# Kernel optimization log

Hardware: AMD Instinct MI355X
Metric: run time of the kernel (lower is better)

The kernel has to match this reference:

```python
import jax, jax.numpy as jnp
import numpy as np

H, W = 256, 256
DX, DY = 1.0, 1.0
EI, KC, GC = 1.0, 1.0, 1.0
LAYERS = [2, 256, 512, 1024, H * W]
B = 64


def _d2x(f, dx):
    # reflect-pad width 1 on x (last axis), stencil [1, -2, 1]
    p = jnp.pad(f, ((0, 0), (0, 0), (0, 0), (1, 1)), mode='reflect')
    return (p[..., :-2] - 2.0 * p[..., 1:-1] + p[..., 2:]) / (dx * dx)


def _d2y(f, dy):
    p = jnp.pad(f, ((0, 0), (0, 0), (1, 1), (0, 0)), mode='reflect')
    return (p[:, :, :-2, :] - 2.0 * p[:, :, 1:-1, :] + p[:, :, 2:, :]) / (dy * dy)


def setup_inputs() -> dict:
    key = jax.random.key(0)
    ks = jax.random.split(key, 10)
    inp = {
        'x_coloc': jax.random.normal(ks[0], (B, LAYERS[0]), jnp.float32),
        'P': jax.random.normal(ks[1], (B, H * W), jnp.float32),
    }
    for i in range(4):
        inp[f'W{i + 1}'] = jax.random.normal(ks[2 + i], (LAYERS[i], LAYERS[i + 1]), jnp.float32) / np.sqrt(LAYERS[i]).astype(np.float32)
        inp[f'b{i + 1}'] = jnp.zeros((LAYERS[i + 1],), jnp.float32)
    return inp


def reference(x_coloc, P, W1, b1, W2, b2, W3, b3, W4, b4):
    # MLP field predictor: Linear+ReLU x3, final Linear -> [B, H*W]
    h = jax.nn.relu(x_coloc @ W1 + b1)
    h = jax.nn.relu(h @ W2 + b2)
    h = jax.nn.relu(h @ W3 + b3)
    f = h @ W4 + b4                      # [B, H*W]
    fm = f.reshape(B, 1, H, W)

    fx2 = _d2x(fm, DX)                   # d2/dx2
    fy2 = _d2y(fm, DY)                   # d2/dy2
    lap = fx2 + fy2
    biharmonic = _d2x(lap, DX) + _d2y(lap, DY)

    residual = EI * biharmonic + GC * (fx2 + fy2) + KC * fm - P.reshape(B, 1, H, W)
    return residual.reshape(B, H * W)
```

## Files before the change

kernel.cpp:

```cpp
#include <hip/hip_runtime.h>
#include <hip/hip_bf16.h>


#define BATCH 64
#define NPIX 65536

typedef __attribute__((ext_vector_type(8))) short short8_t;
typedef __attribute__((ext_vector_type(4))) float f32x4;

__device__ __forceinline__ short f2bf(float x) {
    __hip_bfloat16 h = __float2bfloat16(x);
    short s;
    __builtin_memcpy(&s, &h, 2);
    return s;
}

__global__ void k_layer12(const float* __restrict__ x, const float* __restrict__ W1,
                          const float* __restrict__ b1, const float* __restrict__ W2,
                          const float* __restrict__ b2, float* __restrict__ h2) {
    __shared__ float As[16][64];
    __shared__ float Ws[64][16];
    int tid = threadIdx.x;
    int tn = tid & 15, tm = tid >> 4;
    int n0 = blockIdx.x * 16, m0 = blockIdx.y * 16;
    float acc = 0.f;
    for (int k0 = 0; k0 < 256; k0 += 64) {
#pragma unroll
        for (int j = 0; j < 4; ++j) {
            int e = j * 256 + tid;
            int m = m0 + (e >> 6), kk = k0 + (e & 63);
            float v = x[m * 2 + 0] * W1[kk] + x[m * 2 + 1] * W1[256 + kk] + b1[kk];
            As[e >> 6][e & 63] = v > 0.f ? v : 0.f;
        }
#pragma unroll
        for (int j = 0; j < 4; ++j) {
            int e = j * 256 + tid;
            Ws[e >> 4][e & 15] = W2[(k0 + (e >> 4)) * 512 + n0 + (e & 15)];
        }
        __syncthreads();
#pragma unroll
        for (int k = 0; k < 64; ++k)
            acc += As[tm][k] * Ws[k][tn];
        __syncthreads();
    }
    acc += b2[n0 + tn];
    acc = acc > 0.f ? acc : 0.f;
    h2[(m0 + tm) * 512 + n0 + tn] = acc;
}

__global__ void k_layer3(const float* __restrict__ A, const float* __restrict__ Wt,
                         const float* __restrict__ bias, short* __restrict__ out_bf) {
    __shared__ float As[16][64];
    __shared__ float Ws[64][16];
    int tid = threadIdx.x;
    int tn = tid & 15, tm = tid >> 4;
    int n0 = blockIdx.x * 16, m0 = blockIdx.y * 16;
    float acc = 0.f;
    for (int k0 = 0; k0 < 512; k0 += 64) {
#pragma unroll
        for (int j = 0; j < 4; ++j) {
            int e = j * 256 + tid;
            As[e >> 6][e & 63] = A[(m0 + (e >> 6)) * 512 + k0 + (e & 63)];
        }
#pragma unroll
        for (int j = 0; j < 4; ++j) {
            int e = j * 256 + tid;
            Ws[e >> 4][e & 15] = Wt[(k0 + (e >> 4)) * 1024 + n0 + (e & 15)];
        }
        __syncthreads();
#pragma unroll
        for (int k = 0; k < 64; ++k)
            acc += As[tm][k] * Ws[k][tn];
        __syncthreads();
    }
    acc += bias[n0 + tn];
    acc = acc > 0.f ? acc : 0.f;
    out_bf[(m0 + tm) * 1024 + n0 + tn] = f2bf(acc);
}

__global__ __launch_bounds__(256) void k_gemm_mfma(
        const short* __restrict__ A,
        const float* __restrict__ W,
        const float* __restrict__ bias,
        float* __restrict__ f) {
    __shared__ float Wt[2][32 * 128];
    __shared__ short At[2][4 * 64 * 8];
    const int tid = threadIdx.x;
    const int w = tid >> 6;
    const int lane = tid & 63;
    const int lr = lane & 15;
    const int g = lane >> 4;
    const int n0 = blockIdx.x * 128;

    f32x4 acc[4][2];
#pragma unroll
    for (int a = 0; a < 4; ++a)
#pragma unroll
        for (int b = 0; b < 2; ++b)
            acc[a][b] = {0.f, 0.f, 0.f, 0.f};

    auto stage = [&](int b, int s) {
#pragma unroll
        for (int i = 0; i < 4; ++i) {
            int c = i * 256 + tid;
            int k = c >> 5;
            int q4 = (c & 31) * 4;
            int csw = q4 ^ (((k >> 3) & 1) << 4);
            const float* src = W + (size_t)(s * 32 + k) * NPIX + n0 + csw;
            __builtin_amdgcn_global_load_lds(
                (const __attribute__((address_space(1))) void*)src,
                (__attribute__((address_space(3))) void*)((char*)&Wt[b][0] + c * 16),
                16, 0, 0);
        }
        {
            int kq = tid >> 6;
            int ms = tid & 63;
            int md = ms ^ (kq << 2);
            const short* asrc = A + md * 1024 + s * 32 + kq * 8;
            __builtin_amdgcn_global_load_lds(
                (const __attribute__((address_space(1))) void*)asrc,
                (__attribute__((address_space(3))) void*)((char*)&At[b][0] + tid * 16),
                16, 0, 0);
        }
    };

    stage(0, 0);

    for (int s = 0; s < 32; ++s) {
        const int cur = s & 1;
        if (s < 31) {
            stage(cur ^ 1, s + 1);
            asm volatile("s_waitcnt vmcnt(5)" ::: "memory");
        } else {
            asm volatile("s_waitcnt vmcnt(0)" ::: "memory");
        }
        __builtin_amdgcn_sched_barrier(0);
        __builtin_amdgcn_s_barrier();
        __builtin_amdgcn_sched_barrier(0);

        short8_t afr[4];
#pragma unroll
        for (int mt = 0; mt < 4; ++mt) {
            int mrow = mt * 16 + lr;
            afr[mt] = *(const short8_t*)((const short*)&At[cur][0] +
                                         g * 512 + (mrow ^ (g << 2)) * 8);
        }
#pragma unroll
        for (int t = 0; t < 2; ++t) {
            const int col = w * 32 + t * 16 + lr;
            const int csw = col ^ ((g & 1) << 4);
            short8_t bfr;
#pragma unroll
            for (int j = 0; j < 8; ++j)
                bfr[j] = f2bf(Wt[cur][(g * 8 + j) * 128 + csw]);
#pragma unroll
            for (int mt = 0; mt < 4; ++mt)
                acc[mt][t] = __builtin_amdgcn_mfma_f32_16x16x32_bf16(afr[mt], bfr, acc[mt][t], 0, 0, 0);
        }
        __builtin_amdgcn_s_barrier();
    }

    __syncthreads();
    float* Cl = (float*)&Wt[0][0];
#pragma unroll
    for (int t = 0; t < 2; ++t) {
        const int colb = w * 32 + t * 16 + lr;
        float bb = bias[n0 + colb];
#pragma unroll
        for (int mt = 0; mt < 4; ++mt)
#pragma unroll
            for (int r = 0; r < 4; ++r)
                Cl[(mt * 16 + g * 4 + r) * 128 + colb] = acc[mt][t][r] + bb;
    }
    __syncthreads();
#pragma unroll
    for (int it = 0; it < 8; ++it) {
        int row = (tid >> 5) + it * 8;
        int cc = (tid & 31) * 4;
        f32x4 v = *(const f32x4*)&Cl[row * 128 + cc];
        *(f32x4*)(f + (size_t)row * NPIX + n0 + cc) = v;
    }
}

#define ROWS 16
__device__ __forceinline__ int rfl(int i) {
    return i < 0 ? -i : (i > 255 ? 510 - i : i);
}
__global__ void k_stencil(const float* __restrict__ f, const float* __restrict__ P,
                          float* __restrict__ out) {
    __shared__ float fs[ROWS + 4][256];
    __shared__ float ls[ROWS + 2][256];
    int x = threadIdx.x;
    int y0 = blockIdx.x * ROWS;
    int b = blockIdx.y;
    const float* fb = f + (size_t)b * NPIX;
#pragma unroll
    for (int t = 0; t < ROWS + 4; ++t) {
        int gy = rfl(y0 - 2 + t);
        fs[t][x] = fb[gy * 256 + x];
    }
    __syncthreads();

    int xm = x == 0 ? 1 : x - 1;
    int xp = x == 255 ? 254 : x + 1;

#pragma unroll
    for (int t = 0; t < ROWS + 2; ++t) {
        int jj = rfl(y0 - 1 + t);
        int s  = jj - y0 + 2;
        int sm = rfl(jj - 1) - y0 + 2;
        int sp = rfl(jj + 1) - y0 + 2;
        float c = fs[s][x];
        ls[t][x] = (fs[sm][x] - 2.f * c + fs[sp][x]) +
                   (fs[s][xm] - 2.f * c + fs[s][xp]);
    }
    __syncthreads();

#pragma unroll
    for (int r = 0; r < ROWS; ++r) {
        int y = y0 + r;
        float lc = ls[r + 1][x];
        float bih = (ls[r][x] - 2.f * lc + ls[r + 2][x]) +
                    (ls[r + 1][xm] - 2.f * lc + ls[r + 1][xp]);
        float fc = fs[r + 2][x];
        size_t idx = (size_t)b * NPIX + y * 256 + x;
        out[idx] = bih + lc + fc - P[idx];
    }
}

extern "C" void kernel_launch(void* const* d_in, const int* in_sizes, int n_in,
                              void* d_out, int out_size, void* d_ws, size_t ws_size,
                              hipStream_t stream) {
    const float* x  = (const float*)d_in[0];
    const float* P  = (const float*)d_in[1];
    const float* W1 = (const float*)d_in[2];
    const float* b1 = (const float*)d_in[3];
    const float* W2 = (const float*)d_in[4];
    const float* b2 = (const float*)d_in[5];
    const float* W3 = (const float*)d_in[6];
    const float* b3 = (const float*)d_in[7];
    const float* W4 = (const float*)d_in[8];
    const float* b4 = (const float*)d_in[9];
    float* out = (float*)d_out;

    char* ws = (char*)d_ws;
    float* h2  = (float*)(ws);
    short* h3b = (short*)(ws + (128 << 10));
    float* f   = (float*)(ws + (256 << 10));

    k_layer12<<<dim3(512 / 16, 4), 256, 0, stream>>>(x, W1, b1, W2, b2, h2);
    k_layer3<<<dim3(1024 / 16, 4), 256, 0, stream>>>(h2, W3, b3, h3b);
    k_gemm_mfma<<<NPIX / 128, 256, 0, stream>>>(h3b, W4, b4, f);
    k_stencil<<<dim3(256 / ROWS, BATCH), 256, 0, stream>>>(f, P, out);
}
```

Before: 81.97 us.

## Load A fragments directly to registers and double K-step in W4 GEMM

The large W4 GEMM kernel stops staging the bf16 activation tile through LDS and instead loads A fragments straight from global memory into registers, with a next-step register buffer. The K step per pipeline stage is doubled to 64, halving the number of iterations and barriers, and each stage is split into two halves with finer vmcnt waits so compute on the first half can start while the second half's W loads are still landing. This adds register pressure and doubles LDS use for W, which may reduce occupancy.

After: 88.28 us. 1.08x slower.

```diff
diff --git a/kernel.cpp b/kernel.cpp
--- a/kernel.cpp
+++ b/kernel.cpp
@@ -83,8 +83,7 @@
         const float* __restrict__ W,
         const float* __restrict__ bias,
         float* __restrict__ f) {
-    __shared__ float Wt[2][32 * 128];
-    __shared__ short At[2][4 * 64 * 8];
+    __shared__ float Wt[2][64 * 128];
     const int tid = threadIdx.x;
     const int w = tid >> 6;
     const int lane = tid & 63;
@@ -99,68 +98,89 @@
         for (int b = 0; b < 2; ++b)
             acc[a][b] = {0.f, 0.f, 0.f, 0.f};
 
-    auto stage = [&](int b, int s) {
-#pragma unroll
-        for (int i = 0; i < 4; ++i) {
+    const short* ap = A + lr * 1024 + g * 8;
+    short8_t aC[4][2], aN[4][2];
+
+    auto loadA = [&](short8_t (&dst)[4][2], int s) {
+#pragma unroll
+        for (int mt = 0; mt < 4; ++mt)
+#pragma unroll
+            for (int ks = 0; ks < 2; ++ks)
+                dst[mt][ks] = *(const short8_t*)(ap + mt * 16384 + s * 64 + ks * 32);
+    };
+
+    auto stageW = [&](int b, int s, int ilo, int ihi) {
+#pragma unroll
+        for (int i = 0; i < 8; ++i) {
+            if (i < ilo || i >= ihi) continue;
             int c = i * 256 + tid;
             int k = c >> 5;
             int q4 = (c & 31) * 4;
             int csw = q4 ^ (((k >> 3) & 1) << 4);
-            const float* src = W + (size_t)(s * 32 + k) * NPIX + n0 + csw;
+            const float* src = W + (size_t)(s * 64 + k) * NPIX + n0 + csw;
             __builtin_amdgcn_global_load_lds(
                 (const __attribute__((address_space(1))) void*)src,
                 (__attribute__((address_space(3))) void*)((char*)&Wt[b][0] + c * 16),
                 16, 0, 0);
         }
-        {
-            int kq = tid >> 6;
-            int ms = tid & 63;
-            int md = ms ^ (kq << 2);
-            const short* asrc = A + md * 1024 + s * 32 + kq * 8;
-            __builtin_amdgcn_global_load_lds(
-                (const __attribute__((address_space(1))) void*)asrc,
-                (__attribute__((address_space(3))) void*)((char*)&At[b][0] + tid * 16),
-                16, 0, 0);
-        }
     };
 
-    stage(0, 0);
-
-    for (int s = 0; s < 32; ++s) {
+    auto computeHalf = [&](int cur, int ks, short8_t (&aa)[4][2]) {
+#pragma unroll
+        for (int t = 0; t < 2; ++t) {
+            const int csw = (w * 32 + t * 16 + lr) ^ ((g & 1) << 4);
+            short8_t bfr;
+#pragma unroll
+            for (int j = 0; j < 8; ++j)
+                bfr[j] = f2bf(Wt[cur][(ks * 32 + g * 8 + j) * 128 + csw]);
+#pragma unroll
+            for (int mt = 0; mt < 4; ++mt)
+                acc[mt][t] = __builtin_amdgcn_mfma_f32_16x16x32_bf16(aa[mt][ks], bfr, acc[mt][t], 0, 0, 0);
+        }
+    };
+
+    loadA(aC, 0);
+    __builtin_amdgcn_sched_barrier(0);
+    stageW(0, 0, 0, 8);
+    __builtin_amdgcn_sched_barrier(0);
+
+    for (int s = 0; s < 16; ++s) {
         const int cur = s & 1;
-        if (s < 31) {
-            stage(cur ^ 1, s + 1);
-            asm volatile("s_waitcnt vmcnt(5)" ::: "memory");
+        if (s < 15) {
+            loadA(aN, s + 1);
+            __builtin_amdgcn_sched_barrier(0);
+            stageW(cur ^ 1, s + 1, 0, 4);
+            __builtin_amdgcn_sched_barrier(0);
+            stageW(cur ^ 1, s + 1, 4, 8);
+            __builtin_amdgcn_sched_barrier(0);
+            asm volatile("s_waitcnt vmcnt(20)" ::: "memory");
         } else {
+            asm volatile("s_waitcnt vmcnt(4)" ::: "memory");
+        }
+        __builtin_amdgcn_sched_barrier(0);
+        __builtin_amdgcn_s_barrier();
+        __builtin_amdgcn_sched_barrier(0);
+        computeHalf(cur, 0, aC);
+        if (s < 15)
+            asm volatile("s_waitcnt vmcnt(16)" ::: "memory");
+        else
             asm volatile("s_waitcnt vmcnt(0)" ::: "memory");
-        }
         __builtin_amdgcn_sched_barrier(0);
         __builtin_amdgcn_s_barrier();
         __builtin_amdgcn_sched_barrier(0);
-
-        short8_t afr[4];
-#pragma unroll
-        for (int mt = 0; mt < 4; ++mt) {
-            int mrow = mt * 16 + lr;
-            afr[mt] = *(const short8_t*)((const short*)&At[cur][0] +
-                                         g * 512 + (mrow ^ (g << 2)) * 8);
-        }
-#pragma unroll
-        for (int t = 0; t < 2; ++t) {
-            const int col = w * 32 + t * 16 + lr;
-            const int csw = col ^ ((g & 1) << 4);
-            short8_t bfr;
-#pragma unroll
-            for (int j = 0; j < 8; ++j)
-                bfr[j] = f2bf(Wt[cur][(g * 8 + j) * 128 + csw]);
+        computeHalf(cur, 1, aC);
+        if (s < 15) {
 #pragma unroll
             for (int mt = 0; mt < 4; ++mt)
-                acc[mt][t] = __builtin_amdgcn_mfma_f32_16x16x32_bf16(afr[mt], bfr, acc[mt][t], 0, 0, 0);
-        }
+#pragma unroll
+                for (int ks = 0; ks < 2; ++ks)
+                    aC[mt][ks] = aN[mt][ks];
+        }
+        __builtin_amdgcn_sched_barrier(0);
         __builtin_amdgcn_s_barrier();
-    }
-
-    __syncthreads();
+        __builtin_amdgcn_sched_barrier(0);
+    }
+
     float* Cl = (float*)&Wt[0][0];
 #pragma unroll
     for (int t = 0; t < 2; ++t) {
```
